# Kernel tuning notes

Hardware: AMD Instinct MI355X
Metric: run time of the kernel (lower is better)

Reference implementation:

```python
import jax, jax.numpy as jnp
import numpy as np

NUM_TABLES = 26
ROWS = 100000
EMB = 64
B = 4096
L = 32  # num_lookups per bag
BOT = [256, 512, 256, 64]
TOP = [EMB * (1 + NUM_TABLES), 512, 256, 1]


def _mlp_params(key, dims):
    params = []
    for i in range(len(dims) - 1):
        din, dout = dims[i], dims[i + 1]
        kw, kb, key = jax.random.split(key, 3)
        sw = np.sqrt(2.0 / (din + dout)).astype(np.float32)
        sb = np.sqrt(1.0 / dout).astype(np.float32)
        params.append((jax.random.normal(kw, (dout, din), jnp.float32) * sw,
                       jax.random.normal(kb, (dout,), jnp.float32) * sb))
    return params


def setup_inputs() -> dict:
    key = jax.random.key(0)
    k0, k1, k2, k3, k4 = jax.random.split(key, 5)
    inp = {}
    inp["x_dense"] = jax.random.normal(k0, (B, BOT[0]), jnp.float32)
    inp["x_indices"] = jax.random.randint(k1, (NUM_TABLES, B, L), 0, ROWS)
    bound = np.sqrt(1.0 / ROWS).astype(np.float32)
    inp["emb_tables"] = jax.random.uniform(k2, (NUM_TABLES, ROWS, EMB), jnp.float32, -bound, bound)
    for i, (w, b) in enumerate(_mlp_params(k3, BOT)):
        inp[f"bot_w{i}"] = w
        inp[f"bot_b{i}"] = b
    for i, (w, b) in enumerate(_mlp_params(k4, TOP)):
        inp[f"top_w{i}"] = w
        inp[f"top_b{i}"] = b
    return inp


def _forward(x_dense, x_indices, emb_tables, bot, top):
    # bottom MLP: Linear+ReLU per layer
    h = x_dense
    for w, b in bot:
        h = jax.nn.relu(h @ w.T + b)
    # multi-table EmbeddingBag(mode='sum'): gather rows then sum over bag dim
    # pooled: [T, B, E]
    pooled = jax.vmap(lambda tbl, idx: jnp.take(tbl, idx, axis=0).sum(axis=1))(emb_tables, x_indices)
    emb = jnp.transpose(pooled, (1, 0, 2)).reshape(x_dense.shape[0], -1)  # [B, T*E]
    z = jnp.concatenate([h, emb], axis=1)  # [B, E*(1+T)]
    # top MLP: ReLU on all but last, sigmoid on last
    n = len(top)
    for i, (w, b) in enumerate(top):
        z = z @ w.T + b
        z = jax.nn.sigmoid(z) if i == n - 1 else jax.nn.relu(z)
    return z


def reference(x_dense, x_indices, emb_tables,
              bot_w0, bot_b0, bot_w1, bot_b1, bot_w2, bot_b2,
              top_w0, top_b0, top_w1, top_b1, top_w2, top_b2):
    bot = [(bot_w0, bot_b0), (bot_w1, bot_b1), (bot_w2, bot_b2)]
    top = [(top_w0, top_b0), (top_w1, top_b1), (top_w2, top_b2)]
    return _forward(x_dense, x_indices, emb_tables, bot, top)
```

## Files before the change

kernel.cpp:

```cpp
#include <hip/hip_runtime.h>
#include <hip/hip_bf16.h>
#include <math.h>

typedef __attribute__((ext_vector_type(8))) short short8;
typedef __attribute__((ext_vector_type(4))) float f32x4;

#define NUM_TABLES 26
#define ROWS 100000
#define EMB 64
#define BATCH 4096
#define LOOKUPS 32
#define ZDIM 1728

#define CAST_BLOCKS 128
#define BOT_BLOCKS 256
#define EMBED_BLOCKS (NUM_TABLES * BATCH / 4)

__device__ __forceinline__ unsigned short f2bf(float f) {
  unsigned int u = __float_as_uint(f);
  u += 0x7FFFu + ((u >> 16) & 1u);
  return (unsigned short)(u >> 16);
}
__device__ __forceinline__ float bf2f(unsigned short h) {
  return __uint_as_float(((unsigned int)h) << 16);
}

__device__ __forceinline__ void gload16(const void* g, void* l) {
  __builtin_amdgcn_global_load_lds(
      (const __attribute__((address_space(1))) void*)g,
      (__attribute__((address_space(3))) void*)l, 16, 0, 0);
}

__device__ __forceinline__ short8 wfrag_f32(const float* __restrict__ W, int K,
                                            int colbase, int l, int kc) {
  const float* p = W + (size_t)(colbase + (l & 15)) * K + kc * 32 + ((l >> 4) << 3);
  float4 u = *(const float4*)p;
  float4 v = *(const float4*)(p + 4);
  short8 f;
  f[0] = (short)f2bf(u.x); f[1] = (short)f2bf(u.y);
  f[2] = (short)f2bf(u.z); f[3] = (short)f2bf(u.w);
  f[4] = (short)f2bf(v.x); f[5] = (short)f2bf(v.y);
  f[6] = (short)f2bf(v.z); f[7] = (short)f2bf(v.w);
  return f;
}

struct MegaArgs {
  const float* cast_s[2];
  unsigned short* cast_d[2];
  int cast_n4[2];
  int cast_total;
  const float* x_dense;
  const float* bw0; const float* bb0;
  const float* bw1; const float* bb1;
  const float* bw2; const float* bb2;
  const int* idx;
  const float* tables;
  unsigned short* z;
};

__global__ void mega(MegaArgs a) {
  __shared__ unsigned short xb[16][256];
  __shared__ unsigned short h0[16][512];

  if (blockIdx.x < CAST_BLOCKS) {
    for (int i = blockIdx.x * blockDim.x + threadIdx.x; i < a.cast_total;
         i += CAST_BLOCKS * blockDim.x) {
      int r = i;
      #pragma unroll
      for (int sg = 0; sg < 2; ++sg) {
        if (r < a.cast_n4[sg]) {
          float4 v = ((const float4*)a.cast_s[sg])[r];
          ushort4 o;
          o.x = f2bf(v.x); o.y = f2bf(v.y); o.z = f2bf(v.z); o.w = f2bf(v.w);
          ((ushort4*)a.cast_d[sg])[r] = o;
          break;
        }
        r -= a.cast_n4[sg];
      }
    }
    return;
  }

  if (blockIdx.x < CAST_BLOCKS + BOT_BLOCKS) {
    int b0 = (int)(blockIdx.x - CAST_BLOCKS) << 4;
    int w = threadIdx.x >> 6;
    int l = threadIdx.x & 63;

    #pragma unroll
    for (int i = 0; i < 4; ++i) {
      int flat = i * 256 + threadIdx.x;
      int row = flat >> 6;
      int c4 = flat & 63;
      float4 v = *(const float4*)(a.x_dense + (size_t)(b0 + row) * 256 + c4 * 4);
      int chunk = c4 >> 1;
      int scol = ((chunk ^ (row & 7)) << 3) | ((c4 & 1) << 2);
      ushort4 o;
      o.x = f2bf(v.x); o.y = f2bf(v.y); o.z = f2bf(v.z); o.w = f2bf(v.w);
      *(ushort4*)&xb[row][scol] = o;
    }
    __syncthreads();

    int arow = l & 15;
    int sA = arow & 7;
    const char* xbp = (const char*)&xb[0][0];
    const char* h0p = (const char*)&h0[0][0];

    f32x4 acc0[8];
    #pragma unroll
    for (int n = 0; n < 8; ++n) acc0[n] = (f32x4){0.f, 0.f, 0.f, 0.f};
    for (int kc = 0; kc < 8; ++kc) {
      int c = kc * 4 + (l >> 4);
      short8 av = *(const short8*)(xbp + arow * 512 + ((c ^ sA) << 4));
      #pragma unroll
      for (int n = 0; n < 8; ++n) {
        short8 bv = wfrag_f32(a.bw0, 256, w * 128 + n * 16, l, kc);
        acc0[n] = __builtin_amdgcn_mfma_f32_16x16x32_bf16(av, bv, acc0[n], 0, 0, 0);
      }
    }
    #pragma unroll
    for (int n = 0; n < 8; ++n) {
      int col = w * 128 + n * 16 + (l & 15);
      float bv = a.bb0[col];
      int chunk = col >> 3;
      #pragma unroll
      for (int r = 0; r < 4; ++r) {
        int row = ((l >> 4) << 2) + r;
        float val = acc0[n][r] + bv;
        val = val > 0.f ? val : 0.f;
        h0[row][((chunk ^ (row & 7)) << 3) | (col & 7)] = f2bf(val);
      }
    }
    __syncthreads();

    f32x4 acc1[4];
    #pragma unroll
    for (int n = 0; n < 4; ++n) acc1[n] = (f32x4){0.f, 0.f, 0.f, 0.f};
    for (int kc = 0; kc < 16; ++kc) {
      int c = kc * 4 + (l >> 4);
      short8 av = *(const short8*)(h0p + arow * 1024 + ((c ^ sA) << 4));
      #pragma unroll
      for (int n = 0; n < 4; ++n) {
        short8 bv = wfrag_f32(a.bw1, 512, w * 64 + n * 16, l, kc);
        acc1[n] = __builtin_amdgcn_mfma_f32_16x16x32_bf16(av, bv, acc1[n], 0, 0, 0);
      }
    }
    __syncthreads();
    #pragma unroll
    for (int n = 0; n < 4; ++n) {
      int col = w * 64 + n * 16 + (l & 15);
      float bv = a.bb1[col];
      int chunk = col >> 3;
      #pragma unroll
      for (int r = 0; r < 4; ++r) {
        int row = ((l >> 4) << 2) + r;
        float val = acc1[n][r] + bv;
        val = val > 0.f ? val : 0.f;
        xb[row][((chunk ^ (row & 7)) << 3) | (col & 7)] = f2bf(val);
      }
    }
    __syncthreads();

    f32x4 acc2 = (f32x4){0.f, 0.f, 0.f, 0.f};
    for (int kc = 0; kc < 8; ++kc) {
      int c = kc * 4 + (l >> 4);
      short8 av = *(const short8*)(xbp + arow * 512 + ((c ^ sA) << 4));
      short8 bv = wfrag_f32(a.bw2, 256, w * 16, l, kc);
      acc2 = __builtin_amdgcn_mfma_f32_16x16x32_bf16(av, bv, acc2, 0, 0, 0);
    }
    {
      int col = w * 16 + (l & 15);
      float bv = a.bb2[col];
      #pragma unroll
      for (int r = 0; r < 4; ++r) {
        int row = ((l >> 4) << 2) + r;
        float val = acc2[r] + bv;
        val = val > 0.f ? val : 0.f;
        a.z[(size_t)(b0 + row) * ZDIM + col] = f2bf(val);
      }
    }
    return;
  }

  int g = (int)(((blockIdx.x - CAST_BLOCKS - BOT_BLOCKS) << 2) + (threadIdx.x >> 6));
  int lane = threadIdx.x & 63;
  int t = g >> 12;
  int b = g & 4095;
  const int* ip = a.idx + ((size_t)t * BATCH + b) * LOOKUPS;
  int myidx = (lane < LOOKUPS) ? ip[lane] : 0;
  const float* tbl = a.tables + (size_t)t * ROWS * EMB;
  int grp = lane >> 4;
  int e4 = lane & 15;
  float4 acc = {0.f, 0.f, 0.f, 0.f};
  #pragma unroll
  for (int it = 0; it < 8; ++it) {
    int r = __shfl(myidx, it * 4 + grp, 64);
    float4 v = ((const float4*)(tbl + (size_t)r * EMB))[e4];
    acc.x += v.x; acc.y += v.y; acc.z += v.z; acc.w += v.w;
  }
  #pragma unroll
  for (int m = 16; m <= 32; m <<= 1) {
    acc.x += __shfl_xor(acc.x, m, 64);
    acc.y += __shfl_xor(acc.y, m, 64);
    acc.z += __shfl_xor(acc.z, m, 64);
    acc.w += __shfl_xor(acc.w, m, 64);
  }
  if (lane < 16) {
    ushort4 o;
    o.x = f2bf(acc.x); o.y = f2bf(acc.y); o.z = f2bf(acc.z); o.w = f2bf(acc.w);
    *(ushort4*)&a.z[(size_t)b * ZDIM + EMB + t * EMB + e4 * 4] = o;
  }
}

template<int ACT>
__global__ __launch_bounds__(256) void gemm64s(
    const unsigned short* __restrict__ A,
    const unsigned short* __restrict__ W,
    const float* __restrict__ bias,
    unsigned short* __restrict__ C,
    int M, int N, int K, int ldc) {
  __shared__ unsigned short lds[2][64][64];

  int t = threadIdx.x;
  int lane = t & 63;
  int wid = t >> 6;
  int wr = wid >> 1;
  int wc = wid & 1;

  int ntn = N >> 6;
  int tm = blockIdx.x / ntn;
  int tn = blockIdx.x - tm * ntn;

  int srow = lane >> 3;
  int schunk = (lane & 7) ^ (srow & 7);
  const unsigned short* Ap0 = A + (size_t)(tm * 64 + wid * 16 + srow) * K + schunk * 8;
  const unsigned short* Wp0 = W + (size_t)(tn * 64 + wid * 16 + srow) * K + schunk * 8;
  size_t rowK8 = (size_t)8 * K;

  f32x4 acc[2][2];
  #pragma unroll
  for (int m = 0; m < 2; ++m)
    #pragma unroll
    for (int n = 0; n < 2; ++n)
      acc[m][n] = (f32x4){0.f, 0.f, 0.f, 0.f};

  int ra = wr * 32 + (lane & 15);
  int rb = wc * 32 + (lane & 15);
  int cidx = lane >> 4;
  int sA = ra & 7, sB = rb & 7;

  for (int k0 = 0; k0 < K; k0 += 64) {
    #pragma unroll
    for (int j = 0; j < 2; ++j) {
      gload16(Ap0 + (size_t)k0 + j * rowK8, &lds[0][wid * 16 + j * 8][0]);
      gload16(Wp0 + (size_t)k0 + j * rowK8, &lds[1][wid * 16 + j * 8][0]);
    }
    __syncthreads();

    const char* bA = (const char*)&lds[0][0][0];
    const char* bB = (const char*)&lds[1][0][0];
    #pragma unroll
    for (int kc = 0; kc < 2; ++kc) {
      int c = kc * 4 + cidx;
      short8 a0 = *(const short8*)(bA + ra * 128 + ((c ^ sA) << 4));
      short8 a1 = *(const short8*)(bA + (ra + 16) * 128 + ((c ^ sA) << 4));
      short8 b0 = *(const short8*)(bB + rb * 128 + ((c ^ sB) << 4));
      short8 b1 = *(const short8*)(bB + (rb + 16) * 128 + ((c ^ sB) << 4));
      acc[0][0] = __builtin_amdgcn_mfma_f32_16x16x32_bf16(a0, b0, acc[0][0], 0, 0, 0);
      acc[0][1] = __builtin_amdgcn_mfma_f32_16x16x32_bf16(a0, b1, acc[0][1], 0, 0, 0);
      acc[1][0] = __builtin_amdgcn_mfma_f32_16x16x32_bf16(a1, b0, acc[1][0], 0, 0, 0);
      acc[1][1] = __builtin_amdgcn_mfma_f32_16x16x32_bf16(a1, b1, acc[1][1], 0, 0, 0);
    }
    __syncthreads();
  }

  #pragma unroll
  for (int m = 0; m < 2; ++m) {
    int drow = tm * 64 + wr * 32 + m * 16 + ((lane >> 4) << 2);
    #pragma unroll
    for (int n = 0; n < 2; ++n) {
      int dcol = tn * 64 + wc * 32 + n * 16 + (lane & 15);
      float bv = bias[dcol];
      #pragma unroll
      for (int r = 0; r < 4; ++r) {
        float v = acc[m][n][r] + bv;
        if (ACT == 1) v = v > 0.f ? v : 0.f;
        C[(size_t)(drow + r) * ldc + dcol] = f2bf(v);
      }
    }
  }
}

__global__ void final_layer(const unsigned short* __restrict__ z2,
                            const float* __restrict__ w,
                            const float* __restrict__ bias,
                            float* __restrict__ out) {
  int g = (int)((blockIdx.x * blockDim.x + threadIdx.x) >> 6);
  int lane = threadIdx.x & 63;
  const unsigned short* zp = z2 + (size_t)g * 256;
  float s = 0.f;
  #pragma unroll
  for (int k = 0; k < 256; k += 64)
    s += bf2f(zp[k + lane]) * w[k + lane];
  #pragma unroll
  for (int off = 32; off > 0; off >>= 1)
    s += __shfl_down(s, off, 64);
  if (lane == 0) out[g] = 1.f / (1.f + expf(-(s + bias[0])));
}

extern "C" void kernel_launch(void* const* d_in, const int* in_sizes, int n_in,
                              void* d_out, int out_size, void* d_ws, size_t ws_size,
                              hipStream_t stream) {
  const float* x_dense = (const float*)d_in[0];
  const int*   x_idx   = (const int*)d_in[1];
  const float* tables  = (const float*)d_in[2];
  const float* bw0 = (const float*)d_in[3];  const float* bb0 = (const float*)d_in[4];
  const float* bw1 = (const float*)d_in[5];  const float* bb1 = (const float*)d_in[6];
  const float* bw2 = (const float*)d_in[7];  const float* bb2 = (const float*)d_in[8];
  const float* tw0 = (const float*)d_in[9];  const float* tb0 = (const float*)d_in[10];
  const float* tw1 = (const float*)d_in[11]; const float* tb1 = (const float*)d_in[12];
  const float* tw2 = (const float*)d_in[13]; const float* tb2 = (const float*)d_in[14];
  float* out = (float*)d_out;

  char* ws = (char*)d_ws;
  size_t off = 0;
  auto alloc = [&](size_t bytes) { void* p = ws + off; off += (bytes + 255) & ~(size_t)255; return p; };
  unsigned short* tw0b = (unsigned short*)alloc((size_t)512 * ZDIM * 2);
  unsigned short* tw1b = (unsigned short*)alloc((size_t)256 * 512 * 2);
  unsigned short* z    = (unsigned short*)alloc((size_t)BATCH * ZDIM * 2);
  unsigned short* z1   = (unsigned short*)alloc((size_t)BATCH * 512 * 2);
  unsigned short* z2   = (unsigned short*)alloc((size_t)BATCH * 256 * 2);

  {
    MegaArgs a;
    a.cast_s[0] = tw0; a.cast_d[0] = tw0b; a.cast_n4[0] = 512 * ZDIM / 4;
    a.cast_s[1] = tw1; a.cast_d[1] = tw1b; a.cast_n4[1] = 256 * 512 / 4;
    a.cast_total = a.cast_n4[0] + a.cast_n4[1];
    a.x_dense = x_dense;
    a.bw0 = bw0; a.bb0 = bb0;
    a.bw1 = bw1; a.bb1 = bb1;
    a.bw2 = bw2; a.bb2 = bb2;
    a.idx = x_idx;
    a.tables = tables;
    a.z = z;
    mega<<<CAST_BLOCKS + BOT_BLOCKS + EMBED_BLOCKS, 256, 0, stream>>>(a);
  }

  auto gemm = [&](const unsigned short* A, const unsigned short* W, const float* bias,
                  unsigned short* C, int M, int N, int K, int ldc, int relu) {
    int blocks = (M >> 6) * (N >> 6);
    if (relu)
      gemm64s<1><<<blocks, 256, 0, stream>>>(A, W, bias, C, M, N, K, ldc);
    else
      gemm64s<0><<<blocks, 256, 0, stream>>>(A, W, bias, C, M, N, K, ldc);
  };

  gemm(z,  tw0b, tb0, z1, BATCH, 512, ZDIM, 512, 1);
  gemm(z1, tw1b, tb1, z2, BATCH, 256, 512, 256, 1);

  final_layer<<<BATCH / 4, 256, 0, stream>>>(z2, tw2, tb2, out);
}
```

Before: 177.1 us.

## Fuse second top GEMM with final layer and enlarge first GEMM tile

Replaces the generic 64x64 GEMM for the first top layer with a specialized kernel using 128x64 tiles, so each wave computes 4x2 MFMA tiles and reuses each B fragment across more A rows. The second top GEMM, its ReLU, the 256-to-1 dot product and the sigmoid are merged into one kernel that reads weights directly from global memory. This removes the z2 intermediate buffer and one kernel launch. The cost is only 256 blocks for the first GEMM and un-staged global weight loads in the fused kernel.

```diff
diff --git a/kernel.cpp b/kernel.cpp
--- a/kernel.cpp
+++ b/kernel.cpp
@@ -211,14 +211,14 @@
   }
 }
 
-template<int ACT>
-__global__ __launch_bounds__(256) void gemm64s(
+__global__ __launch_bounds__(256) void gemm_top0(
     const unsigned short* __restrict__ A,
     const unsigned short* __restrict__ W,
     const float* __restrict__ bias,
-    unsigned short* __restrict__ C,
-    int M, int N, int K, int ldc) {
-  __shared__ unsigned short lds[2][64][64];
+    unsigned short* __restrict__ C) {
+  const int K = ZDIM, ldc = 512;
+  __shared__ unsigned short ldsA[128][64];
+  __shared__ unsigned short ldsB[64][64];
 
   int t = threadIdx.x;
   int lane = t & 63;
@@ -226,56 +226,56 @@
   int wr = wid >> 1;
   int wc = wid & 1;
 
-  int ntn = N >> 6;
-  int tm = blockIdx.x / ntn;
-  int tn = blockIdx.x - tm * ntn;
+  int tm = blockIdx.x >> 3;
+  int tn = blockIdx.x & 7;
 
   int srow = lane >> 3;
-  int schunk = (lane & 7) ^ (srow & 7);
-  const unsigned short* Ap0 = A + (size_t)(tm * 64 + wid * 16 + srow) * K + schunk * 8;
+  int schunk = (lane & 7) ^ srow;
+  const unsigned short* Ap0 = A + (size_t)(tm * 128 + wid * 32 + srow) * K + schunk * 8;
   const unsigned short* Wp0 = W + (size_t)(tn * 64 + wid * 16 + srow) * K + schunk * 8;
   size_t rowK8 = (size_t)8 * K;
 
-  f32x4 acc[2][2];
-  #pragma unroll
-  for (int m = 0; m < 2; ++m)
+  f32x4 acc[4][2];
+  #pragma unroll
+  for (int m = 0; m < 4; ++m)
     #pragma unroll
     for (int n = 0; n < 2; ++n)
       acc[m][n] = (f32x4){0.f, 0.f, 0.f, 0.f};
 
-  int ra = wr * 32 + (lane & 15);
   int rb = wc * 32 + (lane & 15);
   int cidx = lane >> 4;
-  int sA = ra & 7, sB = rb & 7;
+  int sB = rb & 7;
 
   for (int k0 = 0; k0 < K; k0 += 64) {
     #pragma unroll
-    for (int j = 0; j < 2; ++j) {
-      gload16(Ap0 + (size_t)k0 + j * rowK8, &lds[0][wid * 16 + j * 8][0]);
-      gload16(Wp0 + (size_t)k0 + j * rowK8, &lds[1][wid * 16 + j * 8][0]);
-    }
-    __syncthreads();
-
-    const char* bA = (const char*)&lds[0][0][0];
-    const char* bB = (const char*)&lds[1][0][0];
+    for (int j = 0; j < 4; ++j)
+      gload16(Ap0 + (size_t)k0 + j * rowK8, &ldsA[wid * 32 + j * 8][0]);
+    #pragma unroll
+    for (int j = 0; j < 2; ++j)
+      gload16(Wp0 + (size_t)k0 + j * rowK8, &ldsB[wid * 16 + j * 8][0]);
+    __syncthreads();
+
+    const char* bA = (const char*)&ldsA[0][0];
+    const char* bB = (const char*)&ldsB[0][0];
     #pragma unroll
     for (int kc = 0; kc < 2; ++kc) {
       int c = kc * 4 + cidx;
-      short8 a0 = *(const short8*)(bA + ra * 128 + ((c ^ sA) << 4));
-      short8 a1 = *(const short8*)(bA + (ra + 16) * 128 + ((c ^ sA) << 4));
       short8 b0 = *(const short8*)(bB + rb * 128 + ((c ^ sB) << 4));
-      short8 b1 = *(const short8*)(bB + (rb + 16) * 128 + ((c ^ sB) << 4));
-      acc[0][0] = __builtin_amdgcn_mfma_f32_16x16x32_bf16(a0, b0, acc[0][0], 0, 0, 0);
-      acc[0][1] = __builtin_amdgcn_mfma_f32_16x16x32_bf16(a0, b1, acc[0][1], 0, 0, 0);
-      acc[1][0] = __builtin_amdgcn_mfma_f32_16x16x32_bf16(a1, b0, acc[1][0], 0, 0, 0);
-      acc[1][1] = __builtin_amdgcn_mfma_f32_16x16x32_bf16(a1, b1, acc[1][1], 0, 0, 0);
-    }
-    __syncthreads();
-  }
-
-  #pragma unroll
-  for (int m = 0; m < 2; ++m) {
-    int drow = tm * 64 + wr * 32 + m * 16 + ((lane >> 4) << 2);
+      short8 b1 = *(const short8*)(bB + (rb + 16) * 128 + ((c ^ ((rb + 16) & 7)) << 4));
+      #pragma unroll
+      for (int m = 0; m < 4; ++m) {
+        int ra = wr * 64 + m * 16 + (lane & 15);
+        short8 av = *(const short8*)(bA + ra * 128 + ((c ^ (ra & 7)) << 4));
+        acc[m][0] = __builtin_amdgcn_mfma_f32_16x16x32_bf16(av, b0, acc[m][0], 0, 0, 0);
+        acc[m][1] = __builtin_amdgcn_mfma_f32_16x16x32_bf16(av, b1, acc[m][1], 0, 0, 0);
+      }
+    }
+    __syncthreads();
+  }
+
+  #pragma unroll
+  for (int m = 0; m < 4; ++m) {
+    int drow = tm * 128 + wr * 64 + m * 16 + ((lane >> 4) << 2);
     #pragma unroll
     for (int n = 0; n < 2; ++n) {
       int dcol = tn * 64 + wc * 32 + n * 16 + (lane & 15);
@@ -283,28 +283,66 @@
       #pragma unroll
       for (int r = 0; r < 4; ++r) {
         float v = acc[m][n][r] + bv;
-        if (ACT == 1) v = v > 0.f ? v : 0.f;
+        v = v > 0.f ? v : 0.f;
         C[(size_t)(drow + r) * ldc + dcol] = f2bf(v);
       }
     }
   }
 }
 
-__global__ void final_layer(const unsigned short* __restrict__ z2,
-                            const float* __restrict__ w,
-                            const float* __restrict__ bias,
-                            float* __restrict__ out) {
-  int g = (int)((blockIdx.x * blockDim.x + threadIdx.x) >> 6);
-  int lane = threadIdx.x & 63;
-  const unsigned short* zp = z2 + (size_t)g * 256;
-  float s = 0.f;
-  #pragma unroll
-  for (int k = 0; k < 256; k += 64)
-    s += bf2f(zp[k + lane]) * w[k + lane];
-  #pragma unroll
-  for (int off = 32; off > 0; off >>= 1)
-    s += __shfl_down(s, off, 64);
-  if (lane == 0) out[g] = 1.f / (1.f + expf(-(s + bias[0])));
+__global__ __launch_bounds__(256) void topfin(
+    const unsigned short* __restrict__ z1,
+    const unsigned short* __restrict__ w1,
+    const float* __restrict__ b1,
+    const float* __restrict__ w2,
+    const float* __restrict__ b2,
+    float* __restrict__ out) {
+  int l = threadIdx.x & 63;
+  int wid = threadIdx.x >> 6;
+  int row0 = (int)blockIdx.x * 64 + wid * 16;
+
+  f32x4 acc[16];
+  #pragma unroll
+  for (int n = 0; n < 16; ++n) acc[n] = (f32x4){0.f, 0.f, 0.f, 0.f};
+
+  const unsigned short* ap0 = z1 + (size_t)(row0 + (l & 15)) * 512 + ((l >> 4) << 3);
+  #pragma unroll 2
+  for (int kc = 0; kc < 16; ++kc) {
+    short8 av = *(const short8*)(ap0 + kc * 32);
+    #pragma unroll
+    for (int n = 0; n < 16; ++n) {
+      const unsigned short* bp = w1 + (size_t)(n * 16 + (l & 15)) * 512 + kc * 32 + ((l >> 4) << 3);
+      short8 bv = *(const short8*)bp;
+      acc[n] = __builtin_amdgcn_mfma_f32_16x16x32_bf16(av, bv, acc[n], 0, 0, 0);
+    }
+  }
+
+  float s0 = 0.f, s1 = 0.f, s2 = 0.f, s3 = 0.f;
+  #pragma unroll
+  for (int n = 0; n < 16; ++n) {
+    int col = n * 16 + (l & 15);
+    float bv = b1[col];
+    float wv = w2[col];
+    float v0 = acc[n][0] + bv; v0 = v0 > 0.f ? v0 : 0.f; s0 += v0 * wv;
+    float v1 = acc[n][1] + bv; v1 = v1 > 0.f ? v1 : 0.f; s1 += v1 * wv;
+    float v2 = acc[n][2] + bv; v2 = v2 > 0.f ? v2 : 0.f; s2 += v2 * wv;
+    float v3 = acc[n][3] + bv; v3 = v3 > 0.f ? v3 : 0.f; s3 += v3 * wv;
+  }
+  #pragma unroll
+  for (int m = 1; m <= 8; m <<= 1) {
+    s0 += __shfl_xor(s0, m, 64);
+    s1 += __shfl_xor(s1, m, 64);
+    s2 += __shfl_xor(s2, m, 64);
+    s3 += __shfl_xor(s3, m, 64);
+  }
+  if ((l & 15) == 0) {
+    int r0 = row0 + (l >> 4) * 4;
+    float bb = b2[0];
+    out[r0 + 0] = 1.f / (1.f + expf(-(s0 + bb)));
+    out[r0 + 1] = 1.f / (1.f + expf(-(s1 + bb)));
+    out[r0 + 2] = 1.f / (1.f + expf(-(s2 + bb)));
+    out[r0 + 3] = 1.f / (1.f + expf(-(s3 + bb)));
+  }
 }
 
 extern "C" void kernel_launch(void* const* d_in, const int* in_sizes, int n_in,
@@ -328,7 +366,6 @@
   unsigned short* tw1b = (unsigned short*)alloc((size_t)256 * 512 * 2);
   unsigned short* z    = (unsigned short*)alloc((size_t)BATCH * ZDIM * 2);
   unsigned short* z1   = (unsigned short*)alloc((size_t)BATCH * 512 * 2);
-  unsigned short* z2   = (unsigned short*)alloc((size_t)BATCH * 256 * 2);
 
   {
     MegaArgs a;
@@ -345,17 +382,7 @@
     mega<<<CAST_BLOCKS + BOT_BLOCKS + EMBED_BLOCKS, 256, 0, stream>>>(a);
   }
 
-  auto gemm = [&](const unsigned short* A, const unsigned short* W, const float* bias,
-                  unsigned short* C, int M, int N, int K, int ldc, int relu) {
-    int blocks = (M >> 6) * (N >> 6);
-    if (relu)
-      gemm64s<1><<<blocks, 256, 0, stream>>>(A, W, bias, C, M, N, K, ldc);
-    else
-      gemm64s<0><<<blocks, 256, 0, stream>>>(A, W, bias, C, M, N, K, ldc);
-  };
-
-  gemm(z,  tw0b, tb0, z1, BATCH, 512, ZDIM, 512, 1);
-  gemm(z1, tw1b, tb1, z2, BATCH, 256, 512, 256, 1);
-
-  final_layer<<<BATCH / 4, 256, 0, stream>>>(z2, tw2, tb2, out);
-}
+  gemm_top0<<<256, 256, 0, stream>>>(z, tw0b, tb0, z1);
+
+  topfin<<<BATCH / 64, 256, 0, stream>>>(z1, tw1b, tb1, tw2, tb2, out);
+}
```

Result: slower. 205.0 us (+15.8%).

## Fuse second top-MLP layer with final sigmoid layer; swizzle GEMM block order

Applied to the files above, without the earlier changes.

Replaces the second GEMM and the final dot-product kernel with one kernel. It computes z1·W1 with MFMA, applies bias and ReLU, and reduces directly against w2 to produce the sigmoid output, so the z2 intermediate buffer and one launch go away. It also remaps block indices in the first GEMM into 8 interleaved groups, aiming for better cache locality or spread across dies. The fused kernel reads W1 straight from global memory without LDS staging, and each block handles only 16 rows, so W1 is re-read by every block.

```diff
diff --git a/kernel.cpp b/kernel.cpp
--- a/kernel.cpp
+++ b/kernel.cpp
@@ -226,9 +226,13 @@
   int wr = wid >> 1;
   int wc = wid & 1;
 
+  int bid = (int)blockIdx.x;
+  int q = (int)gridDim.x >> 3;
+  int swz = (bid & 7) * q + (bid >> 3);
+
   int ntn = N >> 6;
-  int tm = blockIdx.x / ntn;
-  int tn = blockIdx.x - tm * ntn;
+  int tm = swz / ntn;
+  int tn = swz - tm * ntn;
 
   int srow = lane >> 3;
   int schunk = (lane & 7) ^ (srow & 7);
@@ -290,21 +294,65 @@
   }
 }
 
-__global__ void final_layer(const unsigned short* __restrict__ z2,
-                            const float* __restrict__ w,
-                            const float* __restrict__ bias,
-                            float* __restrict__ out) {
-  int g = (int)((blockIdx.x * blockDim.x + threadIdx.x) >> 6);
-  int lane = threadIdx.x & 63;
-  const unsigned short* zp = z2 + (size_t)g * 256;
-  float s = 0.f;
-  #pragma unroll
-  for (int k = 0; k < 256; k += 64)
-    s += bf2f(zp[k + lane]) * w[k + lane];
-  #pragma unroll
-  for (int off = 32; off > 0; off >>= 1)
-    s += __shfl_down(s, off, 64);
-  if (lane == 0) out[g] = 1.f / (1.f + expf(-(s + bias[0])));
+__global__ __launch_bounds__(256) void topfin256(
+    const unsigned short* __restrict__ z1,
+    const unsigned short* __restrict__ w1,
+    const float* __restrict__ b1,
+    const float* __restrict__ w2,
+    const float* __restrict__ b2,
+    float* __restrict__ out) {
+  __shared__ float red[4][16];
+  int l = threadIdx.x & 63;
+  int w = threadIdx.x >> 6;
+  int row0 = (int)blockIdx.x * 16;
+
+  f32x4 acc[4];
+  #pragma unroll
+  for (int n = 0; n < 4; ++n) acc[n] = (f32x4){0.f, 0.f, 0.f, 0.f};
+
+  const unsigned short* ap0 = z1 + (size_t)(row0 + (l & 15)) * 512 + ((l >> 4) << 3);
+  const unsigned short* bp0 = w1 + (size_t)(w * 64 + (l & 15)) * 512 + ((l >> 4) << 3);
+  #pragma unroll 4
+  for (int kc = 0; kc < 16; ++kc) {
+    short8 av = *(const short8*)(ap0 + kc * 32);
+    #pragma unroll
+    for (int n = 0; n < 4; ++n) {
+      short8 bv = *(const short8*)(bp0 + (size_t)n * 16 * 512 + kc * 32);
+      acc[n] = __builtin_amdgcn_mfma_f32_16x16x32_bf16(av, bv, acc[n], 0, 0, 0);
+    }
+  }
+
+  float s0 = 0.f, s1 = 0.f, s2 = 0.f, s3 = 0.f;
+  #pragma unroll
+  for (int n = 0; n < 4; ++n) {
+    int col = w * 64 + n * 16 + (l & 15);
+    float bv = b1[col];
+    float wv = w2[col];
+    float v0 = acc[n][0] + bv; v0 = v0 > 0.f ? v0 : 0.f; s0 += v0 * wv;
+    float v1 = acc[n][1] + bv; v1 = v1 > 0.f ? v1 : 0.f; s1 += v1 * wv;
+    float v2 = acc[n][2] + bv; v2 = v2 > 0.f ? v2 : 0.f; s2 += v2 * wv;
+    float v3 = acc[n][3] + bv; v3 = v3 > 0.f ? v3 : 0.f; s3 += v3 * wv;
+  }
+  #pragma unroll
+  for (int m = 1; m <= 8; m <<= 1) {
+    s0 += __shfl_xor(s0, m, 64);
+    s1 += __shfl_xor(s1, m, 64);
+    s2 += __shfl_xor(s2, m, 64);
+    s3 += __shfl_xor(s3, m, 64);
+  }
+  if ((l & 15) == 0) {
+    int rbase = (l >> 4) * 4;
+    red[w][rbase + 0] = s0;
+    red[w][rbase + 1] = s1;
+    red[w][rbase + 2] = s2;
+    red[w][rbase + 3] = s3;
+  }
+  __syncthreads();
+  if (threadIdx.x < 16) {
+    float s = red[0][threadIdx.x] + red[1][threadIdx.x] +
+              red[2][threadIdx.x] + red[3][threadIdx.x];
+    out[row0 + threadIdx.x] = 1.f / (1.f + expf(-(s + b2[0])));
+  }
 }
 
 extern "C" void kernel_launch(void* const* d_in, const int* in_sizes, int n_in,
@@ -328,7 +376,6 @@
   unsigned short* tw1b = (unsigned short*)alloc((size_t)256 * 512 * 2);
   unsigned short* z    = (unsigned short*)alloc((size_t)BATCH * ZDIM * 2);
   unsigned short* z1   = (unsigned short*)alloc((size_t)BATCH * 512 * 2);
-  unsigned short* z2   = (unsigned short*)alloc((size_t)BATCH * 256 * 2);
 
   {
     MegaArgs a;
@@ -345,17 +392,7 @@
     mega<<<CAST_BLOCKS + BOT_BLOCKS + EMBED_BLOCKS, 256, 0, stream>>>(a);
   }
 
-  auto gemm = [&](const unsigned short* A, const unsigned short* W, const float* bias,
-                  unsigned short* C, int M, int N, int K, int ldc, int relu) {
-    int blocks = (M >> 6) * (N >> 6);
-    if (relu)
-      gemm64s<1><<<blocks, 256, 0, stream>>>(A, W, bias, C, M, N, K, ldc);
-    else
-      gemm64s<0><<<blocks, 256, 0, stream>>>(A, W, bias, C, M, N, K, ldc);
-  };
-
-  gemm(z,  tw0b, tb0, z1, BATCH, 512, ZDIM, 512, 1);
-  gemm(z1, tw1b, tb1, z2, BATCH, 256, 512, 256, 1);
-
-  final_layer<<<BATCH / 4, 256, 0, stream>>>(z2, tw2, tb2, out);
-}
+  gemm64s<1><<<512, 256, 0, stream>>>(z, tw0b, tb0, z1, BATCH, 512, ZDIM, 512);
+
+  topfin256<<<BATCH / 16, 256, 0, stream>>>(z1, tw1b, tb1, tw2, tb2, out);
+}
```

After: 174.9 us, median of 2. About the same (-1.2%).
